# Kernel optimization log

Hardware: AMD Instinct MI355X
Metric: run time of the kernel (lower is better)

The kernel has to match this reference:

```python
import jax, jax.numpy as jnp
import numpy as np

RES = 0.03
NUM_ROTS = 36
NUM_PROPOSAL = 256
OVERSAMPLE = 4           # fixed-size stand-in for the data-dependent while loop
GX, GY, GZ = 272, 112, 272  # grid covering [-4,4.16] x [-0.2,3.16] x [-4,4.16] at res=0.03
POW = 0.5
SEED_DIST_THRESH = 0.3


def setup_inputs() -> dict:
    key = jax.random.key(0)
    ks = jax.random.split(key, 6)
    N, M = 100000, 1024
    extent = jnp.array([7.0, 3.0, 7.0], jnp.float32)
    offset = jnp.array([-3.5, 0.0, -3.5], jnp.float32)
    pc = jax.random.uniform(ks[0], (N, 3), jnp.float32) * extent + offset
    xyz = jax.random.uniform(ks[1], (N, 3), jnp.float32, minval=-0.3, maxval=0.3)
    scale = jax.random.uniform(ks[2], (N, 3), jnp.float32, minval=0.1, maxval=1.0)
    prob = jax.random.uniform(ks[3], (N,), jnp.float32)
    corners = jnp.array([[-4.0, -0.2, -4.0], [4.16, 3.16, 4.16]], jnp.float32)
    vote_points = jax.random.uniform(ks[4], (M, 3), jnp.float32) * extent + offset
    return dict(pc=pc, xyz=xyz, scale=scale, prob=prob, corners=corners, vote_points=vote_points)


def hough_vote(pc, xyz, scale, prob, corners):
    # Each point casts NUM_ROTS votes: center = pc + R_y(theta) @ xyz_offset
    thetas = 2.0 * jnp.pi * jnp.arange(NUM_ROTS, dtype=jnp.float32) / NUM_ROTS
    c, s = jnp.cos(thetas), jnp.sin(thetas)  # [R]
    ox, oy, oz = xyz[:, 0:1], xyz[:, 1:2], xyz[:, 2:3]  # [N,1]
    rx = ox * c + oz * s      # [N,R]
    rz = -ox * s + oz * c     # [N,R]
    tx = pc[:, 0:1] + rx
    ty = jnp.broadcast_to(pc[:, 1:2] + oy, tx.shape)
    tz = pc[:, 2:3] + rz
    ix = jnp.floor((tx - corners[0, 0]) / RES + 0.5).astype(jnp.int32)
    iy = jnp.floor((ty - corners[0, 1]) / RES + 0.5).astype(jnp.int32)
    iz = jnp.floor((tz - corners[0, 2]) / RES + 0.5).astype(jnp.int32)
    inb = ((ix >= 0) & (ix < GX) & (iy >= 0) & (iy < GY) & (iz >= 0) & (iz < GZ))
    ixc = jnp.clip(ix, 0, GX - 1)
    iyc = jnp.clip(iy, 0, GY - 1)
    izc = jnp.clip(iz, 0, GZ - 1)
    flat = ((ixc * GY + iyc) * GZ + izc).ravel()  # [N*R]
    w = (prob[:, None] * inb.astype(prob.dtype))  # [N,R]
    grid_obj = jnp.zeros((GX * GY * GZ,), pc.dtype).at[flat].add(w.ravel())
    ws = (w[:, :, None] * scale[:, None, :]).reshape(-1, 3)
    grid_scale = jnp.zeros((GX * GY * GZ, 3), pc.dtype).at[flat].add(ws)
    hv_map = grid_obj.reshape(GX, GY, GZ)
    hv_scale = (grid_scale / (grid_obj[:, None] + 1e-7)).reshape(GX, GY, GZ, 3)
    return hv_map, hv_scale


def reference(pc, xyz, scale, prob, corners, vote_points):
    hv_map, hv_scale = hough_vote(pc, xyz, scale, prob, corners)
    hv_map_y = jnp.power(hv_map.max(axis=1) + 1e-7, POW)  # [GX,GZ]
    hv_map_yidx = jnp.argmax(hv_map, axis=1)              # [GX,GZ]
    dist = hv_map_y.reshape(-1)
    finite = jnp.isfinite(dist)
    safe = jnp.where(finite, dist, 0.0)
    ok = finite.all() & (safe.sum() >= 1e-7)
    dist = jnp.where(ok, safe, 1.0)

    # fixed-size oversampling instead of the data-dependent while loop
    K = NUM_PROPOSAL * OVERSAMPLE
    sample = jax.random.categorical(jax.random.key(42), jnp.log(dist + 1e-30), shape=(K,))
    sample_val = dist[sample]
    xi = sample // GZ
    zi = sample % GZ
    yi = hv_map_yidx[xi, zi]
    world_loc = jnp.stack([xi, yi, zi], -1).astype(pc.dtype) * RES + corners[0]  # [K,3]
    sc = hv_scale[xi, yi, zi, :]  # [K,3]

    # min distance to vote seeds; keep candidates near seeds (fallback: keep all)
    d2seed = jnp.min(jnp.linalg.norm(world_loc[:, None, :] - vote_points[None, :, :], axis=-1), axis=-1)
    keep = d2seed < SEED_DIST_THRESH
    keep = jnp.where(keep.any(), keep, jnp.ones_like(keep))
    order = jnp.argsort(jnp.where(keep, 0, 1))  # stable: passing candidates first
    sel = order[:NUM_PROPOSAL]
    candidates = world_loc[sel]
    scales_out = sc[sel]
    probs = jnp.zeros((NUM_PROPOSAL,), pc.dtype)
    return candidates, probs, scales_out
```

## Files before the change

kernel.cpp:

```cpp
#include <hip/hip_runtime.h>
#include <math.h>
#include <stdio.h>
#include <stdint.h>

#define GXD 272
#define GYD 112
#define GZD 272
#define NROT 36
#define CCLS (GXD*GZD)
#define KSMP 1024
#define NPROP 256
#define HSLOTS 2048
#define YH 56
#define NBINS (GXD*2)
#define SLICE (GYD*GZD)
#define SVCAP 64
#define ROWG 16

struct RotTab { float c[NROT]; float s[NROT]; };

__device__ __forceinline__ uint32_t cell_hash(int flat) {
    return ((uint32_t)flat * 2654435761u) >> 21;
}

#define ROTL_AB(x, r) __builtin_amdgcn_alignbit((x), (x), 32u - (r))

__device__ __forceinline__ void threefry2x32(uint32_t k0, uint32_t k1,
                                             uint32_t x0, uint32_t x1,
                                             uint32_t& o0, uint32_t& o1) {
    uint32_t ks2 = k0 ^ k1 ^ 0x1BD11BDAu;
#define TF_ROUND(r) { x0 += x1; x1 = ROTL_AB(x1, r); x1 ^= x0; }
    x0 += k0; x1 += k1;
    TF_ROUND(13) TF_ROUND(15) TF_ROUND(26) TF_ROUND(6)
    x0 += k1;  x1 += ks2 + 1u;
    TF_ROUND(17) TF_ROUND(29) TF_ROUND(16) TF_ROUND(24)
    x0 += ks2; x1 += k0 + 2u;
    TF_ROUND(13) TF_ROUND(15) TF_ROUND(26) TF_ROUND(6)
    x0 += k0;  x1 += k1 + 3u;
    TF_ROUND(17) TF_ROUND(29) TF_ROUND(16) TF_ROUND(24)
    x0 += k1;  x1 += ks2 + 4u;
    TF_ROUND(13) TF_ROUND(15) TF_ROUND(26) TF_ROUND(6)
    x0 += ks2; x1 += k0 + 5u;
#undef TF_ROUND
    o0 = x0; o1 = x1;
}

__device__ __forceinline__ uint32_t tf_bits(uint32_t i) {
    uint32_t o0, o1;
    threefry2x32(0u, 42u, 0u, i, o0, o1);
    return o0 ^ o1;
}

template<int W>
__device__ __forceinline__ void tf_batch(uint32_t ib, uint32_t* out) {
    constexpr uint32_t K1  = 42u;
    constexpr uint32_t KS2 = 0u ^ 42u ^ 0x1BD11BDAu;
    uint32_t x0[W], x1[W];
#pragma unroll
    for (int j = 0; j < W; ++j) {
        x0[j] = 0u;
        x1[j] = ib + (uint32_t)(j * CCLS) + K1;
    }
    constexpr uint32_t R[5][4]  = {{13,15,26,6},{17,29,16,24},{13,15,26,6},
                                   {17,29,16,24},{13,15,26,6}};
    constexpr uint32_t I0[5] = {K1, KS2, 0u, K1, KS2};
    constexpr uint32_t I1[5] = {KS2 + 1u, 2u, K1 + 3u, KS2 + 4u, 5u};
#pragma unroll
    for (int g = 0; g < 5; ++g) {
#pragma unroll
        for (int r = 0; r < 4; ++r) {
#pragma unroll
            for (int j = 0; j < W; ++j) {
                x0[j] += x1[j];
                x1[j] = ROTL_AB(x1[j], R[g][r]);
                x1[j] ^= x0[j];
            }
        }
#pragma unroll
        for (int j = 0; j < W; ++j) { x0[j] += I0[g]; x1[j] += I1[g]; }
    }
#pragma unroll
    for (int j = 0; j < W; ++j) out[j] = x0[j] ^ x1[j];
}

__device__ __forceinline__ float uniform_from_bits(uint32_t b) {
    const float TINY = 1.1754943508222875e-38f;
    float f = __uint_as_float((b >> 9) | 0x3f800000u) - 1.0f;
    float u = __fadd_rn(__fmul_rn(f, 1.0f), TINY);
    return fmaxf(TINY, u);
}

__device__ __forceinline__ float gumbel_from_u(float u) {
    float l1 = (float)log((double)u);
    float l2 = (float)log((double)(-l1));
    return -l2;
}

__device__ __forceinline__ bool vote_iy(float py, float oy, float c0y, int& iy) {
    float ty = __fadd_rn(py, oy);
    float vy = __fadd_rn(__fdiv_rn(__fsub_rn(ty, c0y), 0.03f), 0.5f);
    iy = (int)floorf(vy);
    return (iy >= 0 && iy < GYD);
}
__device__ __forceinline__ bool vote_xz(float px, float pz, float ox, float oz,
                                        float c, float s, float c0x, float c0z,
                                        int& ix, int& iz) {
    float rx = __fadd_rn(__fmul_rn(ox, c), __fmul_rn(oz, s));
    float rz = __fadd_rn(__fmul_rn(-ox, s), __fmul_rn(oz, c));
    float tx = __fadd_rn(px, rx);
    float tz = __fadd_rn(pz, rz);
    float vx = __fadd_rn(__fdiv_rn(__fsub_rn(tx, c0x), 0.03f), 0.5f);
    float vz = __fadd_rn(__fdiv_rn(__fsub_rn(tz, c0z), 0.03f), 0.5f);
    ix = (int)floorf(vx);
    iz = (int)floorf(vz);
    return (ix >= 0 && ix < GXD && iz >= 0 && iz < GZD);
}
__device__ __forceinline__ bool vote_cell(float px, float py, float pz,
                                          float ox, float oy, float oz,
                                          float c, float s,
                                          float c0x, float c0y, float c0z,
                                          int& flat) {
    int iy, ix, iz;
    if (!vote_iy(py, oy, c0y, iy)) return false;
    if (!vote_xz(px, pz, ox, oz, c, s, c0x, c0z, ix, iz)) return false;
    flat = (ix*GYD + iy)*GZD + iz;
    return true;
}

__global__ __launch_bounds__(256) void k_count(const float* __restrict__ pc, const float* __restrict__ xyz,
                          const float* __restrict__ corners, int N, RotTab rt,
                          int* __restrict__ bincnt) {
    __shared__ int h[NBINS];
    int tid = threadIdx.x;
    for (int j = tid; j < NBINS; j += 256) h[j] = 0;
    __syncthreads();
    int i = blockIdx.x * 256 + tid;
    if (i < N) {
        float px = pc[3*i], py = pc[3*i+1], pz = pc[3*i+2];
        float ox = xyz[3*i], oy = xyz[3*i+1], oz = xyz[3*i+2];
        int iy;
        if (vote_iy(py, oy, corners[1], iy)) {
            int ybit = (iy >= YH) ? 1 : 0;
            float c0x = corners[0], c0z = corners[2];
            for (int r = 0; r < NROT; ++r) {
                int ix, iz;
                if (vote_xz(px, pz, ox, oz, rt.c[r], rt.s[r], c0x, c0z, ix, iz))
                    atomicAdd(&h[ix*2 + ybit], 1);
            }
        }
    }
    __syncthreads();
    for (int j = tid; j < NBINS; j += 256) if (h[j]) atomicAdd(&bincnt[j], h[j]);
}

__global__ __launch_bounds__(576) void k_prefix(const int* __restrict__ bincnt,
                         int* __restrict__ binbase, int* __restrict__ bincur) {
    __shared__ int sc[576];
    int tid = threadIdx.x;
    int v = (tid < NBINS) ? bincnt[tid] : 0;
    sc[tid] = v;
    __syncthreads();
    for (int off = 1; off < 576; off <<= 1) {
        int x = sc[tid];
        if (tid >= off) x += sc[tid - off];
        __syncthreads();
        sc[tid] = x;
        __syncthreads();
    }
    if (tid < NBINS) {
        int excl = sc[tid] - v;
        binbase[tid] = excl;
        bincur[tid] = excl;
    }
}

__global__ __launch_bounds__(256) void k_binwrite(const float* __restrict__ pc, const float* __restrict__ xyz,
                          const float* __restrict__ prob, const float* __restrict__ corners,
                          int N, RotTab rt, int* __restrict__ bincur,
                          int* __restrict__ vflat, float* __restrict__ vw) {
    __shared__ int h[NBINS];
    __shared__ int bbase[NBINS];
    int tid = threadIdx.x;
    for (int j = tid; j < NBINS; j += 256) h[j] = 0;
    __syncthreads();
    int i = blockIdx.x * 256 + tid;
    float px=0, py=0, pz=0, ox=0, oy=0, oz=0, w0=0, c0x=0, c0z=0;
    int iy = -1, ybit = 0;
    bool act = false;
    if (i < N) {
        px = pc[3*i]; py = pc[3*i+1]; pz = pc[3*i+2];
        ox = xyz[3*i]; oy = xyz[3*i+1]; oz = xyz[3*i+2];
        w0 = prob[i];
        c0x = corners[0]; c0z = corners[2];
        if (vote_iy(py, oy, corners[1], iy)) {
            act = true;
            ybit = (iy >= YH) ? 1 : 0;
        }
    }
    if (act) {
        for (int r = 0; r < NROT; ++r) {
            int ix, iz;
            if (vote_xz(px, pz, ox, oz, rt.c[r], rt.s[r], c0x, c0z, ix, iz))
                atomicAdd(&h[ix*2 + ybit], 1);
        }
    }
    __syncthreads();
    for (int j = tid; j < NBINS; j += 256) {
        int cnt = h[j];
        bbase[j] = cnt ? atomicAdd(&bincur[j], cnt) : 0;
        h[j] = 0;
    }
    __syncthreads();
    if (act) {
        for (int r = 0; r < NROT; ++r) {
            int ix, iz;
            if (vote_xz(px, pz, ox, oz, rt.c[r], rt.s[r], c0x, c0z, ix, iz)) {
                int bin = ix*2 + ybit;
                int rank = atomicAdd(&h[bin], 1);
                int slot = bbase[bin] + rank;
                vflat[slot] = (ix*GYD + iy)*GZD + iz;
                vw[slot] = w0;
            }
        }
    }
}

__global__ __launch_bounds__(256) void k_accum(const int* __restrict__ binbase,
                          const int* __restrict__ bincnt,
                          const int* __restrict__ vflat, const float* __restrict__ vw,
                          float* __restrict__ gobj) {
    __shared__ float tile[YH*GZD];
    int b = blockIdx.x;
    int x = b >> 1, yh = b & 1;
    int tid = threadIdx.x;
    for (int j = tid; j < YH*GZD; j += 256) tile[j] = 0.0f;
    __syncthreads();
    int lo = binbase[b], n = bincnt[b];
    int xoff = x * SLICE;
    int yoff = yh * (YH*GZD);
    for (int j = lo + tid; j < lo + n; j += 256) {
        int rel = vflat[j] - xoff;
        atomicAdd(&tile[rel - yoff], vw[j]);
    }
    __syncthreads();
    float* dst = gobj + (size_t)xoff + yoff;
    for (int j = tid; j < YH*GZD; j += 256) dst[j] = tile[j];
}

__global__ __launch_bounds__(256) void k_colmax(const float* __restrict__ gobj,
                         float* __restrict__ logits, int* __restrict__ yidx,
                         float* __restrict__ sumdist) {
    int c = blockIdx.x * blockDim.x + threadIdx.x;
    float d = 0.0f;
    if (c < CCLS) {
        int x = c / GZD, z = c % GZD;
        const float* base = gobj + (size_t)x*GYD*GZD + z;
        float m = base[0];
        int mi = 0;
        for (int y = 1; y < GYD; ++y) {
            float v = base[(size_t)y*GZD];
            if (v > m) { m = v; mi = y; }
        }
        d = __fsqrt_rn(__fadd_rn(m, 1e-7f));
        yidx[c] = mi;
        logits[c] = (float)log((double)__fadd_rn(d, 1e-30f));
    }
    __shared__ float sred[256];
    int tid = threadIdx.x;
    sred[tid] = d; __syncthreads();
    for (int off = 128; off > 0; off >>= 1) {
        if (tid < off) sred[tid] += sred[tid+off];
        __syncthreads();
    }
    if (tid == 0) atomicAdd(sumdist, sred[0]);
}

__global__ __launch_bounds__(256) void k_thresh(const float* __restrict__ logits,
                                                const float* __restrict__ sumdist,
                                                uint32_t* __restrict__ bth) {
    int c = blockIdx.x * blockDim.x + threadIdx.x;
    if (c >= CCLS) return;
    double B0 = log((double)*sumdist) - 3.0;
    double t = exp(-exp((double)logits[c] - (B0 - 0.05)));
    long long k_th = (long long)floor(t * 8388608.0) - 2;
    uint32_t b;
    if (k_th <= 0)              b = 0u;
    else if (k_th >= 8388608LL) b = 0xFFFFFFFFu;
    else                        b = (uint32_t)k_th << 9;
    bth[c] = b;
}

__global__ __launch_bounds__(256) void k_prefilter(const uint32_t* __restrict__ bth,
                                                   int* __restrict__ svcnt,
                                                   uint2* __restrict__ svrec) {
    int c = blockIdx.x * 256 + threadIdx.x;
    int k0 = blockIdx.y * (KSMP / ROWG);
    uint32_t th = bth[c];
    uint32_t i = (uint32_t)k0 * (uint32_t)CCLS + (uint32_t)c;
#pragma unroll 1
    for (int kk = 0; kk < KSMP / ROWG; kk += 8) {
        uint32_t b[8];
        tf_batch<8>(i, b);
#pragma unroll
        for (int j = 0; j < 8; ++j) {
            if (__builtin_expect(b[j] >= th, 0)) {
                int row = k0 + kk + j;
                int idx = atomicAdd(&svcnt[row], 1);
                if (idx < SVCAP) svrec[row * SVCAP + idx] = make_uint2((uint32_t)c, b[j]);
            }
        }
        i += 8u * (uint32_t)CCLS;
    }
}

__global__ __launch_bounds__(256) void k_finalize(const float* __restrict__ logits,
                                                  const int* __restrict__ svcnt,
                                                  const uint2* __restrict__ svrec,
                                                  int* __restrict__ samples) {
    int k = blockIdx.x;
    int tid = threadIdx.x;
    int n = svcnt[k];
    float best = -INFINITY; int bc = 0x7fffffff;
    if (n > 0 && n <= SVCAP) {
        if (tid < n) {
            uint2 rec = svrec[k * SVCAP + tid];
            int c = (int)rec.x;
            best = __fadd_rn(gumbel_from_u(uniform_from_bits(rec.y)), logits[c]);
            bc = c;
        }
    } else {
        uint32_t base = (uint32_t)k * (uint32_t)CCLS;
        for (int c = tid; c < CCLS; c += 256) {
            float v = __fadd_rn(gumbel_from_u(uniform_from_bits(tf_bits(base + (uint32_t)c))), logits[c]);
            if (v > best || (v == best && c < bc)) { best = v; bc = c; }
        }
    }
    __shared__ float sv[256];
    __shared__ int   si[256];
    sv[tid] = best; si[tid] = bc; __syncthreads();
    for (int off = 128; off > 0; off >>= 1) {
        if (tid < off) {
            float v2 = sv[tid+off]; int i2 = si[tid+off];
            if (v2 > sv[tid] || (v2 == sv[tid] && i2 < si[tid])) { sv[tid] = v2; si[tid] = i2; }
        }
        __syncthreads();
    }
    if (tid == 0) samples[k] = si[0];
}

__global__ __launch_bounds__(256) void k_build_table(const int* __restrict__ samples,
                                                     const int* __restrict__ yidx,
                                                     int* __restrict__ hkeys,
                                                     float* __restrict__ gsmall) {
    int tid = threadIdx.x;
    for (int j = tid; j < HSLOTS; j += 256) hkeys[j] = -1;
    for (int j = tid; j < 3*HSLOTS; j += 256) gsmall[j] = 0.0f;
    __syncthreads();
    for (int k = tid; k < KSMP; k += 256) {
        int s = samples[k];
        int xi = s / GZD, zi = s % GZD;
        int yi = yidx[s];
        int flat = (xi*GYD + yi)*GZD + zi;
        uint32_t h = cell_hash(flat);
        for (;;) {
            int prev = atomicCAS(&hkeys[h], -1, flat);
            if (prev == -1 || prev == flat) break;
            h = (h + 1) & (HSLOTS - 1);
        }
    }
}

__global__ __launch_bounds__(256) void k_scale_scatter(const float* __restrict__ pc, const float* __restrict__ xyz,
                          const float* __restrict__ scale, const float* __restrict__ prob,
                          const float* __restrict__ corners,
                          const int* __restrict__ hkeys, float* __restrict__ gsmall,
                          int N, RotTab rt) {
    __shared__ int lk[HSLOTS];
    for (int j = threadIdx.x; j < HSLOTS; j += 256) lk[j] = hkeys[j];
    __syncthreads();
    int i = blockIdx.x * blockDim.x + threadIdx.x;
    int r = blockIdx.y;
    if (i >= N) return;
    int flat;
    if (!vote_cell(pc[3*i], pc[3*i+1], pc[3*i+2], xyz[3*i], xyz[3*i+1], xyz[3*i+2],
                   rt.c[r], rt.s[r], corners[0], corners[1], corners[2], flat)) return;
    uint32_t h = cell_hash(flat);
    int slot = -1;
    for (;;) {
        int key = lk[h];
        if (key == flat) { slot = (int)h; break; }
        if (key == -1) break;
        h = (h + 1) & (HSLOTS - 1);
    }
    if (slot < 0) return;
    float w0 = prob[i];
    atomicAdd(&gsmall[3*slot+0], __fmul_rn(w0, scale[3*i]));
    atomicAdd(&gsmall[3*slot+1], __fmul_rn(w0, scale[3*i+1]));
    atomicAdd(&gsmall[3*slot+2], __fmul_rn(w0, scale[3*i+2]));
}

__global__ __launch_bounds__(256) void k_post(const float* __restrict__ gobj,
                       const int* __restrict__ hkeys, const float* __restrict__ gsmall,
                       const int* __restrict__ yidx, const int* __restrict__ samples,
                       const float* __restrict__ corners, const float* __restrict__ vp, int M,
                       float* __restrict__ world, float* __restrict__ scv, int* __restrict__ keep) {
    int k = blockIdx.x;
    int tid = threadIdx.x;
    int s = samples[k];
    int xi = s / GZD, zi = s % GZD;
    int yi = yidx[s];
    float wx = __fadd_rn(__fmul_rn((float)xi, 0.03f), corners[0]);
    float wy = __fadd_rn(__fmul_rn((float)yi, 0.03f), corners[1]);
    float wz = __fadd_rn(__fmul_rn((float)zi, 0.03f), corners[2]);

    float dmin = INFINITY;
    for (int j = tid; j < M; j += 256) {
        float dx = __fsub_rn(wx, vp[3*j]);
        float dy = __fsub_rn(wy, vp[3*j+1]);
        float dz = __fsub_rn(wz, vp[3*j+2]);
        float sq = __fadd_rn(__fadd_rn(__fmul_rn(dx,dx), __fmul_rn(dy,dy)), __fmul_rn(dz,dz));
        dmin = fminf(dmin, __fsqrt_rn(sq));
    }
    __shared__ float sm[256];
    sm[tid] = dmin; __syncthreads();
    for (int off = 128; off > 0; off >>= 1) {
        if (tid < off) sm[tid] = fminf(sm[tid], sm[tid+off]);
        __syncthreads();
    }
    if (tid == 0) {
        world[3*k] = wx; world[3*k+1] = wy; world[3*k+2] = wz;
        int flat = (xi*GYD + yi)*GZD + zi;
        uint32_t h = cell_hash(flat);
        while (hkeys[h] != flat) h = (h + 1) & (HSLOTS - 1);
        float go = __fadd_rn(gobj[flat], 1e-7f);
        scv[3*k+0] = __fdiv_rn(gsmall[3*h+0], go);
        scv[3*k+1] = __fdiv_rn(gsmall[3*h+1], go);
        scv[3*k+2] = __fdiv_rn(gsmall[3*h+2], go);
        keep[k] = (sm[0] < 0.3f) ? 1 : 0;
    }
}

__global__ __launch_bounds__(256) void k_select(const float* __restrict__ world,
                                                const float* __restrict__ scv,
                                                const int* __restrict__ keep,
                                                float* __restrict__ out) {
    __shared__ int kp[KSMP];
    __shared__ int tsum[256];
    __shared__ int sel[NPROP];
    __shared__ int anyk;
    int tid = threadIdx.x;
    if (tid == 0) anyk = 0;
    __syncthreads();
    int a = 0;
    for (int j = tid; j < KSMP; j += 256) { int v = keep[j]; kp[j] = v; a |= v; }
    if (a) anyk = 1;
    __syncthreads();
    int any = anyk;
    int j0 = tid * 4;
    int k0v = any ? kp[j0]   : 1;
    int k1v = any ? kp[j0+1] : 1;
    int k2v = any ? kp[j0+2] : 1;
    int k3v = any ? kp[j0+3] : 1;
    int s0 = k0v, s1 = s0 + k1v, s2 = s1 + k2v, s3 = s2 + k3v;
    tsum[tid] = s3;
    __syncthreads();
    for (int off = 1; off < 256; off <<= 1) {
        int x = tsum[tid];
        if (tid >= off) x += tsum[tid - off];
        __syncthreads();
        tsum[tid] = x;
        __syncthreads();
    }
    int base = (tid > 0) ? tsum[tid-1] : 0;
    int nk = tsum[255];
    int inc[4] = { base + s0, base + s1, base + s2, base + s3 };
    int kv[4]  = { k0v, k1v, k2v, k3v };
    for (int q = 0; q < 4; ++q) {
        int j = j0 + q;
        int slot = kv[q] ? (inc[q] - 1) : (nk + j - inc[q]);
        if (slot < NPROP) sel[slot] = j;
    }
    __syncthreads();
    if (tid < NPROP) {
        int sidx = sel[tid];
        out[3*tid+0] = world[3*sidx+0];
        out[3*tid+1] = world[3*sidx+1];
        out[3*tid+2] = world[3*sidx+2];
        out[3*NPROP + tid] = 0.0f;
        out[4*NPROP + 3*tid + 0] = scv[3*sidx+0];
        out[4*NPROP + 3*tid + 1] = scv[3*sidx+1];
        out[4*NPROP + 3*tid + 2] = scv[3*sidx+2];
    }
}

extern "C" void kernel_launch(void* const* d_in, const int* in_sizes, int n_in,
                              void* d_out, int out_size, void* d_ws, size_t ws_size,
                              hipStream_t stream) {
    const float* pc      = (const float*)d_in[0];
    const float* xyz     = (const float*)d_in[1];
    const float* scale   = (const float*)d_in[2];
    const float* prob    = (const float*)d_in[3];
    const float* corners = (const float*)d_in[4];
    const float* vp      = (const float*)d_in[5];
    int N = in_sizes[0] / 3;
    int M = in_sizes[5] / 3;
    int NV = N * NROT;

    const size_t G = (size_t)GXD * GYD * GZD;
    float* gobj    = (float*)d_ws;
    float* sumdist = gobj + G;
    int*   bincnt  = (int*)(sumdist + 1);
    int*   svcnt   = bincnt + NBINS;
    int*   binbase = svcnt + KSMP;
    int*   bincur  = binbase + NBINS;
    float* logits  = (float*)(bincur + NBINS);
    uint32_t* bth  = (uint32_t*)(logits + CCLS);
    int*   yidx    = (int*)(bth + CCLS);
    int*   samples = yidx + CCLS;
    int*   hkeys   = samples + KSMP;
    float* gsmall  = (float*)(hkeys + HSLOTS);
    float* world   = gsmall + 3*HSLOTS;
    float* scv     = world + 3*KSMP;
    int*   keep    = (int*)(scv + 3*KSMP);
    uint2* svrec   = (uint2*)(((uintptr_t)(keep + KSMP) + 15) & ~(uintptr_t)15);
    int*   vflat   = (int*)(svrec + (size_t)KSMP * SVCAP);
    float* vw      = (float*)(vflat + NV);
    size_t need = (size_t)((char*)(vw + NV) - (char*)d_ws);
    if (ws_size < need) {
        fprintf(stderr, "kernel_launch: ws_size %zu < needed %zu\n", ws_size, need);
        return;
    }

    hipMemsetAsync(sumdist, 0, (1 + NBINS + KSMP)*sizeof(int), stream);

    RotTab rt;
    const float twopi = (float)(2.0 * M_PI);
    for (int r = 0; r < NROT; ++r) {
        float th = (twopi * (float)r) / 36.0f;
        rt.c[r] = (float)cos((double)th);
        rt.s[r] = (float)sin((double)th);
    }

    int pblocks = (N + 255) / 256;
    k_count<<<pblocks, 256, 0, stream>>>(pc, xyz, corners, N, rt, bincnt);
    k_prefix<<<1, 576, 0, stream>>>(bincnt, binbase, bincur);
    k_binwrite<<<pblocks, 256, 0, stream>>>(pc, xyz, prob, corners, N, rt, bincur, vflat, vw);
    k_accum<<<NBINS, 256, 0, stream>>>(binbase, bincnt, vflat, vw, gobj);
    k_colmax<<<(CCLS + 255) / 256, 256, 0, stream>>>(gobj, logits, yidx, sumdist);
    k_thresh<<<(CCLS + 255) / 256, 256, 0, stream>>>(logits, sumdist, bth);
    dim3 pf_grid(CCLS / 256, ROWG);
    k_prefilter<<<pf_grid, 256, 0, stream>>>(bth, svcnt, svrec);
    k_finalize<<<KSMP, 256, 0, stream>>>(logits, svcnt, svrec, samples);
    k_build_table<<<1, 256, 0, stream>>>(samples, yidx, hkeys, gsmall);
    dim3 sgrid(pblocks, NROT);
    k_scale_scatter<<<sgrid, 256, 0, stream>>>(pc, xyz, scale, prob, corners, hkeys, gsmall, N, rt);
    k_post<<<KSMP, 256, 0, stream>>>(gobj, hkeys, gsmall, yidx, samples, corners, vp, M, world, scv, keep);
    k_select<<<1, 256, 0, stream>>>(world, scv, keep, (float*)d_out);
}
```

Measured before the change: 420.7 us.

## Replace binned counting-sort voting with direct global atomic scatter into grid

Removes the four-kernel vote path (count, prefix scan, bin write, per-slice LDS accumulate). In its place, a single kernel over points × rotations adds each vote straight into the global grid with atomicAdd, after a memset of the whole grid. This drops the staging buffers for vote indices and weights and their write-then-read traffic, along with three launches. The cost is millions of scattered global float atomics and an explicit zeroing of the full grid, which the old path did not need because the accumulate kernel wrote every cell itself.

New measurement: 498.1 us. 1.18x slower.

```diff
diff --git a/kernel.cpp b/kernel.cpp
--- a/kernel.cpp
+++ b/kernel.cpp
@@ -11,9 +11,6 @@
 #define KSMP 1024
 #define NPROP 256
 #define HSLOTS 2048
-#define YH 56
-#define NBINS (GXD*2)
-#define SLICE (GYD*GZD)
 #define SVCAP 64
 #define ROWG 16
 
@@ -127,124 +124,16 @@
     return true;
 }
 
-__global__ __launch_bounds__(256) void k_count(const float* __restrict__ pc, const float* __restrict__ xyz,
-                          const float* __restrict__ corners, int N, RotTab rt,
-                          int* __restrict__ bincnt) {
-    __shared__ int h[NBINS];
-    int tid = threadIdx.x;
-    for (int j = tid; j < NBINS; j += 256) h[j] = 0;
-    __syncthreads();
-    int i = blockIdx.x * 256 + tid;
-    if (i < N) {
-        float px = pc[3*i], py = pc[3*i+1], pz = pc[3*i+2];
-        float ox = xyz[3*i], oy = xyz[3*i+1], oz = xyz[3*i+2];
-        int iy;
-        if (vote_iy(py, oy, corners[1], iy)) {
-            int ybit = (iy >= YH) ? 1 : 0;
-            float c0x = corners[0], c0z = corners[2];
-            for (int r = 0; r < NROT; ++r) {
-                int ix, iz;
-                if (vote_xz(px, pz, ox, oz, rt.c[r], rt.s[r], c0x, c0z, ix, iz))
-                    atomicAdd(&h[ix*2 + ybit], 1);
-            }
-        }
-    }
-    __syncthreads();
-    for (int j = tid; j < NBINS; j += 256) if (h[j]) atomicAdd(&bincnt[j], h[j]);
-}
-
-__global__ __launch_bounds__(576) void k_prefix(const int* __restrict__ bincnt,
-                         int* __restrict__ binbase, int* __restrict__ bincur) {
-    __shared__ int sc[576];
-    int tid = threadIdx.x;
-    int v = (tid < NBINS) ? bincnt[tid] : 0;
-    sc[tid] = v;
-    __syncthreads();
-    for (int off = 1; off < 576; off <<= 1) {
-        int x = sc[tid];
-        if (tid >= off) x += sc[tid - off];
-        __syncthreads();
-        sc[tid] = x;
-        __syncthreads();
-    }
-    if (tid < NBINS) {
-        int excl = sc[tid] - v;
-        binbase[tid] = excl;
-        bincur[tid] = excl;
-    }
-}
-
-__global__ __launch_bounds__(256) void k_binwrite(const float* __restrict__ pc, const float* __restrict__ xyz,
-                          const float* __restrict__ prob, const float* __restrict__ corners,
-                          int N, RotTab rt, int* __restrict__ bincur,
-                          int* __restrict__ vflat, float* __restrict__ vw) {
-    __shared__ int h[NBINS];
-    __shared__ int bbase[NBINS];
-    int tid = threadIdx.x;
-    for (int j = tid; j < NBINS; j += 256) h[j] = 0;
-    __syncthreads();
-    int i = blockIdx.x * 256 + tid;
-    float px=0, py=0, pz=0, ox=0, oy=0, oz=0, w0=0, c0x=0, c0z=0;
-    int iy = -1, ybit = 0;
-    bool act = false;
-    if (i < N) {
-        px = pc[3*i]; py = pc[3*i+1]; pz = pc[3*i+2];
-        ox = xyz[3*i]; oy = xyz[3*i+1]; oz = xyz[3*i+2];
-        w0 = prob[i];
-        c0x = corners[0]; c0z = corners[2];
-        if (vote_iy(py, oy, corners[1], iy)) {
-            act = true;
-            ybit = (iy >= YH) ? 1 : 0;
-        }
-    }
-    if (act) {
-        for (int r = 0; r < NROT; ++r) {
-            int ix, iz;
-            if (vote_xz(px, pz, ox, oz, rt.c[r], rt.s[r], c0x, c0z, ix, iz))
-                atomicAdd(&h[ix*2 + ybit], 1);
-        }
-    }
-    __syncthreads();
-    for (int j = tid; j < NBINS; j += 256) {
-        int cnt = h[j];
-        bbase[j] = cnt ? atomicAdd(&bincur[j], cnt) : 0;
-        h[j] = 0;
-    }
-    __syncthreads();
-    if (act) {
-        for (int r = 0; r < NROT; ++r) {
-            int ix, iz;
-            if (vote_xz(px, pz, ox, oz, rt.c[r], rt.s[r], c0x, c0z, ix, iz)) {
-                int bin = ix*2 + ybit;
-                int rank = atomicAdd(&h[bin], 1);
-                int slot = bbase[bin] + rank;
-                vflat[slot] = (ix*GYD + iy)*GZD + iz;
-                vw[slot] = w0;
-            }
-        }
-    }
-}
-
-__global__ __launch_bounds__(256) void k_accum(const int* __restrict__ binbase,
-                          const int* __restrict__ bincnt,
-                          const int* __restrict__ vflat, const float* __restrict__ vw,
-                          float* __restrict__ gobj) {
-    __shared__ float tile[YH*GZD];
-    int b = blockIdx.x;
-    int x = b >> 1, yh = b & 1;
-    int tid = threadIdx.x;
-    for (int j = tid; j < YH*GZD; j += 256) tile[j] = 0.0f;
-    __syncthreads();
-    int lo = binbase[b], n = bincnt[b];
-    int xoff = x * SLICE;
-    int yoff = yh * (YH*GZD);
-    for (int j = lo + tid; j < lo + n; j += 256) {
-        int rel = vflat[j] - xoff;
-        atomicAdd(&tile[rel - yoff], vw[j]);
-    }
-    __syncthreads();
-    float* dst = gobj + (size_t)xoff + yoff;
-    for (int j = tid; j < YH*GZD; j += 256) dst[j] = tile[j];
+__global__ __launch_bounds__(256) void k_vote(const float* __restrict__ pc, const float* __restrict__ xyz,
+                        const float* __restrict__ prob, const float* __restrict__ corners,
+                        int N, RotTab rt, float* __restrict__ gobj) {
+    int i = blockIdx.x * 256 + threadIdx.x;
+    int r = blockIdx.y;
+    if (i >= N) return;
+    int flat;
+    if (!vote_cell(pc[3*i], pc[3*i+1], pc[3*i+2], xyz[3*i], xyz[3*i+1], xyz[3*i+2],
+                   rt.c[r], rt.s[r], corners[0], corners[1], corners[2], flat)) return;
+    atomicAdd(&gobj[flat], prob[i]);
 }
 
 __global__ __launch_bounds__(256) void k_colmax(const float* __restrict__ gobj,
@@ -504,16 +393,12 @@
     const float* vp      = (const float*)d_in[5];
     int N = in_sizes[0] / 3;
     int M = in_sizes[5] / 3;
-    int NV = N * NROT;
 
     const size_t G = (size_t)GXD * GYD * GZD;
     float* gobj    = (float*)d_ws;
     float* sumdist = gobj + G;
-    int*   bincnt  = (int*)(sumdist + 1);
-    int*   svcnt   = bincnt + NBINS;
-    int*   binbase = svcnt + KSMP;
-    int*   bincur  = binbase + NBINS;
-    float* logits  = (float*)(bincur + NBINS);
+    int*   svcnt   = (int*)(sumdist + 1);
+    float* logits  = (float*)(svcnt + KSMP);
     uint32_t* bth  = (uint32_t*)(logits + CCLS);
     int*   yidx    = (int*)(bth + CCLS);
     int*   samples = yidx + CCLS;
@@ -523,15 +408,13 @@
     float* scv     = world + 3*KSMP;
     int*   keep    = (int*)(scv + 3*KSMP);
     uint2* svrec   = (uint2*)(((uintptr_t)(keep + KSMP) + 15) & ~(uintptr_t)15);
-    int*   vflat   = (int*)(svrec + (size_t)KSMP * SVCAP);
-    float* vw      = (float*)(vflat + NV);
-    size_t need = (size_t)((char*)(vw + NV) - (char*)d_ws);
+    size_t need = (size_t)((char*)(svrec + (size_t)KSMP * SVCAP) - (char*)d_ws);
     if (ws_size < need) {
         fprintf(stderr, "kernel_launch: ws_size %zu < needed %zu\n", ws_size, need);
         return;
     }
 
-    hipMemsetAsync(sumdist, 0, (1 + NBINS + KSMP)*sizeof(int), stream);
+    hipMemsetAsync(gobj, 0, (G + 1 + KSMP)*sizeof(float), stream);
 
     RotTab rt;
     const float twopi = (float)(2.0 * M_PI);
@@ -542,10 +425,8 @@
     }
 
     int pblocks = (N + 255) / 256;
-    k_count<<<pblocks, 256, 0, stream>>>(pc, xyz, corners, N, rt, bincnt);
-    k_prefix<<<1, 576, 0, stream>>>(bincnt, binbase, bincur);
-    k_binwrite<<<pblocks, 256, 0, stream>>>(pc, xyz, prob, corners, N, rt, bincur, vflat, vw);
-    k_accum<<<NBINS, 256, 0, stream>>>(binbase, bincnt, vflat, vw, gobj);
+    dim3 vgrid(pblocks, NROT);
+    k_vote<<<vgrid, 256, 0, stream>>>(pc, xyz, prob, corners, N, rt, gobj);
     k_colmax<<<(CCLS + 255) / 256, 256, 0, stream>>>(gobj, logits, yidx, sumdist);
     k_thresh<<<(CCLS + 255) / 256, 256, 0, stream>>>(logits, sumdist, bth);
     dim3 pf_grid(CCLS / 256, ROWG);
```
